# Kernel optimization log

Measured on AMD Instinct MI355X. Metric: run time of the kernel, lower is better.

## Reference

```python
import jax, jax.numpy as jnp
import numpy as np
import math

D_MODEL = 1024
NUM_HEADS = 16
HEAD_DIM = D_MODEL // NUM_HEADS
B, T = 2, 2048


def _linear_params(key, d_in, d_out):
    kw, kb = jax.random.split(key)
    s = 1.0 / math.sqrt(d_in)
    W = jax.random.uniform(kw, (d_in, d_out), jnp.float32, -s, s)
    b = jax.random.uniform(kb, (d_out,), jnp.float32, -s, s)
    return W, b


def setup_inputs() -> dict:
    key = jax.random.key(0)
    ks = jax.random.split(key, 10)
    x_real = jax.random.normal(ks[0], (B, T, D_MODEL), jnp.float32)
    x_imag = jax.random.normal(ks[1], (B, T, D_MODEL), jnp.float32)
    Wqr, bqr = _linear_params(ks[2], D_MODEL, D_MODEL)
    Wqi, bqi = _linear_params(ks[3], D_MODEL, D_MODEL)
    Wkr, bkr = _linear_params(ks[4], D_MODEL, D_MODEL)
    Wki, bki = _linear_params(ks[5], D_MODEL, D_MODEL)
    Wvr, bvr = _linear_params(ks[6], D_MODEL, D_MODEL)
    Wvi, bvi = _linear_params(ks[7], D_MODEL, D_MODEL)
    Wor, bor = _linear_params(ks[8], D_MODEL, D_MODEL)
    Woi, boi = _linear_params(ks[9], D_MODEL, D_MODEL)
    return dict(x_real=x_real, x_imag=x_imag,
                Wqr=Wqr, bqr=bqr, Wqi=Wqi, bqi=bqi,
                Wkr=Wkr, bkr=bkr, Wki=Wki, bki=bki,
                Wvr=Wvr, bvr=bvr, Wvi=Wvi, bvi=bvi,
                Wor=Wor, bor=bor, Woi=Woi, boi=boi)


def _heads(x):
    # (B,T,C) -> (B,H,T,Dh)
    b, t, _ = x.shape
    return x.reshape(b, t, NUM_HEADS, HEAD_DIM).transpose(0, 2, 1, 3)


def reference(x_real, x_imag,
              Wqr, bqr, Wqi, bqi, Wkr, bkr, Wki, bki,
              Wvr, bvr, Wvi, bvi, Wor, bor, Woi, boi):
    b, t, c = x_real.shape
    # NOTE: first two qr/qi assignments in the torch forward are dead code;
    # effective math is below.
    qr = _heads(x_real @ Wqr + bqr)
    qi = _heads(x_imag @ Wqi + bqi)
    kr = _heads(x_real @ Wkr + bkr)
    ki = _heads(x_imag @ Wki + bki)
    vr = _heads(x_real @ Wvr + bvr)
    vi = _heads(x_imag @ Wvi + bvi)
    # Re(Q K^H) score: Qr*Kr + Qi*Ki, scaled
    score = (jnp.einsum('bhtd,bhsd->bhts', qr, kr)
             + jnp.einsum('bhtd,bhsd->bhts', qi, ki)) / math.sqrt(HEAD_DIM)
    causal = jnp.triu(jnp.ones((t, t), dtype=bool), k=1)  # True above diagonal
    score = jnp.where(causal[None, None], -jnp.inf, score)
    attn = jax.nn.softmax(score, axis=-1)
    out_r = jnp.einsum('bhts,bhsd->bhtd', attn, vr).transpose(0, 2, 1, 3).reshape(b, t, c)
    out_i = jnp.einsum('bhts,bhsd->bhtd', attn, vi).transpose(0, 2, 1, 3).reshape(b, t, c)
    final_r = out_r @ Wor + bor
    final_i = out_i @ Woi + boi
    return (final_r, final_i)
```

## Files before the change

kernel.cpp:

```cpp
#include <hip/hip_runtime.h>
#include <hip/hip_bf16.h>


typedef __attribute__((ext_vector_type(8))) __bf16 bf16x8;
typedef __attribute__((ext_vector_type(4))) float f32x4;
typedef unsigned short u16;

#define L2E 1.44269504088896340736f

__device__ __forceinline__ void gl2lds16(const void* g, void* l) {
  __builtin_amdgcn_global_load_lds(
      (const __attribute__((address_space(1))) unsigned int*)g,
      (__attribute__((address_space(3))) unsigned int*)l, 16, 0, 0);
}

__device__ __forceinline__ u16 f2bf(float f) {
  union { float f; unsigned u; } v;
  v.f = f;
  unsigned r = v.u + 0x7FFFu + ((v.u >> 16) & 1u);
  return (u16)(r >> 16);
}

__global__ void cvt_bf16(const float* __restrict__ in, u16* __restrict__ out, int n) {
  int stride = gridDim.x * blockDim.x * 4;
  for (int i = (blockIdx.x * blockDim.x + threadIdx.x) * 4; i < n; i += stride) {
    float4 v = *(const float4*)(in + i);
    ushort4 o;
    o.x = f2bf(v.x); o.y = f2bf(v.y); o.z = f2bf(v.z); o.w = f2bf(v.w);
    *(ushort4*)(out + i) = o;
  }
}

struct WPtrs { const float* w[8]; };

__global__ void cvt_w_t(WPtrs ptrs, u16* __restrict__ out) {
  __shared__ float tile[32][33];
  const float* W = ptrs.w[blockIdx.z];
  u16* o = out + ((size_t)blockIdx.z << 20);
  int tx = threadIdx.x & 31, ty = threadIdx.x >> 5;
  int bx = blockIdx.x * 32, by = blockIdx.y * 32;
#pragma unroll
  for (int k = 0; k < 4; k++) {
    int r = by + ty + k * 8;
    tile[ty + k * 8][tx] = W[(size_t)r * 1024 + bx + tx];
  }
  __syncthreads();
#pragma unroll
  for (int k = 0; k < 4; k++) {
    int n = bx + ty + k * 8;
    o[(size_t)n * 1024 + by + tx] = f2bf(tile[tx][ty + k * 8]);
  }
}

struct GemmArgs {
  const u16* A[6];
  const u16* Wt[6];
  const float* bias[6];
  void* dst[6];
  int off[6];
};

template <int MODE>
__global__ __launch_bounds__(256, 2) void gemm_bf16(GemmArgs args) {
  const int z = blockIdx.z;
  const u16* __restrict__ A = args.A[z];
  const u16* __restrict__ Bt = args.Wt[z];
  const float* __restrict__ bias = args.bias[z];
  const int brow = blockIdx.x * 128;
  const int bcol = blockIdx.y * 128;

  __shared__ u16 lA[2][128 * 32];
  __shared__ u16 lB[2][128 * 32];

  const int tid = threadIdx.x;
  const int w = tid >> 6, lane = tid & 63;
  const int wrow = (w >> 1) * 64, wcol = (w & 1) * 64;

  f32x4 acc[4][4] = {};

  auto stage = [&](int buf, int t) {
    int k0 = t * 32;
#pragma unroll
    for (int s = 0; s < 2; s++) {
      int q = w * 2 + s;
      int lr = q * 16 + (lane >> 2);
      int csrc = (lane & 3) ^ ((lr >> 1) & 3);
      gl2lds16(A + (size_t)(brow + lr) * 1024 + k0 + csrc * 8, &lA[buf][q * 512]);
    }
#pragma unroll
    for (int s = 0; s < 2; s++) {
      int q = w * 2 + s;
      int lr = q * 16 + (lane >> 2);
      int csrc = (lane & 3) ^ ((lr >> 1) & 3);
      gl2lds16(Bt + (size_t)(bcol + lr) * 1024 + k0 + csrc * 8, &lB[buf][q * 512]);
    }
  };

  stage(0, 0);
  __syncthreads();

  int buf = 0;
  for (int t = 0; t < 32; t++) {
    if (t + 1 < 32) stage(buf ^ 1, t + 1);
    bf16x8 a[4], b[4];
#pragma unroll
    for (int i = 0; i < 4; i++) {
      int row = wrow + i * 16 + (lane & 15);
      int cs = (lane >> 4) ^ ((row >> 1) & 3);
      a[i] = *(const bf16x8*)&lA[buf][row * 32 + cs * 8];
      int col = wcol + i * 16 + (lane & 15);
      int cs2 = (lane >> 4) ^ ((col >> 1) & 3);
      b[i] = *(const bf16x8*)&lB[buf][col * 32 + cs2 * 8];
    }
#pragma unroll
    for (int i = 0; i < 4; i++)
#pragma unroll
      for (int j = 0; j < 4; j++)
        acc[i][j] = __builtin_amdgcn_mfma_f32_16x16x32_bf16(a[i], b[j], acc[i][j], 0, 0, 0);
    __syncthreads();
    buf ^= 1;
  }

  const int off = args.off[z];
#pragma unroll
  for (int i = 0; i < 4; i++)
#pragma unroll
    for (int j = 0; j < 4; j++)
#pragma unroll
      for (int r = 0; r < 4; r++) {
        int grow = brow + wrow + i * 16 + (lane >> 4) * 4 + r;
        int gcol = bcol + wcol + j * 16 + (lane & 15);
        float v = acc[i][j][r] + bias[gcol];
        if (MODE == 0) {
          ((float*)args.dst[z])[(size_t)grow * 1024 + gcol] = v;
        } else {
          int bb = grow >> 11, tt = grow & 2047;
          int h = gcol >> 6, dh = gcol & 63;
          ((u16*)args.dst[z])[(((size_t)(bb * 16 + h) * 2048 + tt) << 7) + off + dh] = f2bf(v);
        }
      }
}

__global__ void transpose_v(const u16* __restrict__ Vc, u16* __restrict__ Vt) {
  __shared__ u16 tile[64 * 64];
  const int bh = blockIdx.z, t0 = blockIdx.x * 64, d0 = blockIdx.y * 64;
  const int tid = threadIdx.x;
  const int tl = tid >> 3, c = tid & 7;
#pragma unroll
  for (int hh = 0; hh < 2; hh++) {
    int t = tl + hh * 32;
    int sc = c ^ (t & 7) ^ ((t >> 3) & 7);
    *(bf16x8*)&tile[t * 64 + sc * 8] =
        *(const bf16x8*)&Vc[((size_t)bh * 2048 + t0 + t) * 128 + d0 + c * 8];
  }
  __syncthreads();
#pragma unroll
  for (int hh = 0; hh < 2; hh++) {
    int d = tl + hh * 32;
    bf16x8 v;
#pragma unroll
    for (int j = 0; j < 8; j++) {
      int t = c * 8 + j;
      int sc = (d >> 3) ^ (t & 7) ^ ((t >> 3) & 7);
      v[j] = ((const __bf16*)tile)[t * 64 + sc * 8 + (d & 7)];
    }
    *(bf16x8*)&Vt[((size_t)bh * 128 + d0 + d) * 2048 + t0 + c * 8] = v;
  }
}

__global__ __launch_bounds__(256, 2) void attn_kernel(
    const u16* __restrict__ Q, const u16* __restrict__ K, const u16* __restrict__ Vt,
    u16* __restrict__ Or, u16* __restrict__ Oi) {
  const int bh = blockIdx.x;
  const int ii = (int)gridDim.y - 1 - (int)blockIdx.y;
  const int tid = threadIdx.x, w = tid >> 6, lane = tid & 63;
  const int ql = lane & 15, hi = lane >> 4;
  const int b = bh >> 4, h = bh & 15;

  __shared__ u16 lK[2][64 * 128];
  __shared__ u16 lV[2][128 * 64];
  __shared__ u16 lP[4][16 * 64];

  const int qrow0 = ii * 64 + w * 16;
  const int q = qrow0 + ql;

  bf16x8 qf[4];
#pragma unroll
  for (int kk = 0; kk < 4; kk++)
    qf[kk] = *(const bf16x8*)(Q + ((size_t)bh * 2048 + q) * 128 + kk * 32 + hi * 8);

  f32x4 o[8] = {};
  float m = -__builtin_inff(), l = 0.f;

  const int ntiles = ii + 1;

  auto stageKV = [&](int buf, int jt) {
#pragma unroll
    for (int s = 0; s < 4; s++) {
      int seg = w * 4 + s;
      int srow = seg * 4 + (lane >> 4);
      int csrc = (lane & 15) ^ (srow & 15);
      gl2lds16(K + ((size_t)bh * 2048 + jt * 64 + srow) * 128 + csrc * 8, &lK[buf][seg * 512]);
    }
#pragma unroll
    for (int s = 0; s < 4; s++) {
      int seg = w * 4 + s;
      int dv = seg * 8 + (lane >> 3);
      int csrc = (lane & 7) ^ (dv & 7);
      gl2lds16(Vt + ((size_t)bh * 128 + dv) * 2048 + jt * 64 + csrc * 8, &lV[buf][seg * 512]);
    }
  };

  stageKV(0, 0);
  __syncthreads();

  int buf = 0;
  for (int jt = 0; jt < ntiles; jt++) {
    if (jt + 1 < ntiles) stageKV(buf ^ 1, jt + 1);

    f32x4 s[4] = {};
#pragma unroll
    for (int kk = 0; kk < 4; kk++) {
#pragma unroll
      for (int j = 0; j < 4; j++) {
        int sl = j * 16 + ql;
        int cs = (kk * 4 + hi) ^ (sl & 15);
        bf16x8 kf = *(const bf16x8*)&lK[buf][sl * 128 + cs * 8];
        s[j] = __builtin_amdgcn_mfma_f32_16x16x32_bf16(kf, qf[kk], s[j], 0, 0, 0);
      }
    }

    const bool diag = (jt == ii);
    float mx = -__builtin_inff();
#pragma unroll
    for (int j = 0; j < 4; j++)
#pragma unroll
      for (int r = 0; r < 4; r++) {
        float v = s[j][r] * 0.125f;
        if (diag) {
          int kg = jt * 64 + j * 16 + hi * 4 + r;
          if (kg > q) v = -__builtin_inff();
        }
        s[j][r] = v;
        mx = fmaxf(mx, v);
      }
    mx = fmaxf(mx, __shfl_xor(mx, 16));
    mx = fmaxf(mx, __shfl_xor(mx, 32));

    if (__any(mx > m + 8.f)) {
      float mn = fmaxf(m, mx);
      float alpha = exp2f((m - mn) * L2E);
      l *= alpha;
#pragma unroll
      for (int jv = 0; jv < 8; jv++) o[jv] *= alpha;
      m = mn;
    }

    float rs = 0.f;
    unsigned pk[4][2];
#pragma unroll
    for (int j = 0; j < 4; j++) {
      float p0 = exp2f((s[j][0] - m) * L2E);
      float p1 = exp2f((s[j][1] - m) * L2E);
      float p2 = exp2f((s[j][2] - m) * L2E);
      float p3 = exp2f((s[j][3] - m) * L2E);
      rs += (p0 + p1) + (p2 + p3);
      pk[j][0] = (unsigned)f2bf(p0) | ((unsigned)f2bf(p1) << 16);
      pk[j][1] = (unsigned)f2bf(p2) | ((unsigned)f2bf(p3) << 16);
    }
    rs += __shfl_xor(rs, 16);
    rs += __shfl_xor(rs, 32);
    l += rs;

#pragma unroll
    for (int j = 0; j < 4; j++) {
      int byte_off = ql * 128 + ((j * 32 + hi * 8) ^ ((ql & 7) << 4));
      *(uint2*)((char*)&lP[w][0] + byte_off) = make_uint2(pk[j][0], pk[j][1]);
    }
    asm volatile("s_waitcnt lgkmcnt(0)" ::: "memory");
    __builtin_amdgcn_sched_barrier(0);

#pragma unroll
    for (int kks = 0; kks < 2; kks++) {
      int pb = ql * 128 + ((kks * 64 + hi * 16) ^ ((ql & 7) << 4));
      bf16x8 pf = *(const bf16x8*)((char*)&lP[w][0] + pb);
#pragma unroll
      for (int jv = 0; jv < 8; jv++) {
        int dv = jv * 16 + ql;
        int cs = (kks * 4 + hi) ^ (dv & 7);
        bf16x8 vf = *(const bf16x8*)&lV[buf][dv * 64 + cs * 8];
        o[jv] = __builtin_amdgcn_mfma_f32_16x16x32_bf16(vf, pf, o[jv], 0, 0, 0);
      }
    }

    __syncthreads();
    buf ^= 1;
  }

  float linv = 1.f / l;
  const size_t obase = ((size_t)b * 2048 + q) * 1024 + h * 64;
#pragma unroll
  for (int jv = 0; jv < 8; jv++) {
    ushort4 st;
    st.x = f2bf(o[jv][0] * linv);
    st.y = f2bf(o[jv][1] * linv);
    st.z = f2bf(o[jv][2] * linv);
    st.w = f2bf(o[jv][3] * linv);
    u16* dst = (jv < 4) ? Or : Oi;
    *(ushort4*)(dst + obase + (jv & 3) * 16 + hi * 4) = st;
  }
}

extern "C" void kernel_launch(void* const* d_in, const int* in_sizes, int n_in,
                              void* d_out, int out_size, void* d_ws, size_t ws_size,
                              hipStream_t stream) {
  (void)in_sizes; (void)n_in; (void)out_size; (void)ws_size;

  const float* x_real = (const float*)d_in[0];
  const float* x_imag = (const float*)d_in[1];

  char* ws = (char*)d_ws;
  size_t off = 0;
  auto alloc = [&](size_t bytes) {
    void* p = ws + off;
    off += (bytes + 255) & ~(size_t)255;
    return p;
  };
  const size_t MK = 4096ull * 1024;
  u16* xr16 = (u16*)alloc(MK * 2);
  u16* xi16 = (u16*)alloc(MK * 2);
  u16* Wt   = (u16*)alloc(8ull * 1024 * 1024 * 2);
  u16* Qc   = (u16*)alloc(32ull * 2048 * 128 * 2);
  u16* Kc   = (u16*)alloc(32ull * 2048 * 128 * 2);
  u16* Vc   = (u16*)alloc(32ull * 2048 * 128 * 2);
  u16* Vt   = (u16*)alloc(32ull * 2048 * 128 * 2);
  u16* Or   = Vc;
  u16* Oi   = Vc + MK;

  cvt_bf16<<<2048, 256, 0, stream>>>(x_real, xr16, (int)MK);
  cvt_bf16<<<2048, 256, 0, stream>>>(x_imag, xi16, (int)MK);

  WPtrs wp;
  wp.w[0] = (const float*)d_in[2];
  wp.w[1] = (const float*)d_in[4];
  wp.w[2] = (const float*)d_in[6];
  wp.w[3] = (const float*)d_in[8];
  wp.w[4] = (const float*)d_in[10];
  wp.w[5] = (const float*)d_in[12];
  wp.w[6] = (const float*)d_in[14];
  wp.w[7] = (const float*)d_in[16];
  cvt_w_t<<<dim3(32, 32, 8), 256, 0, stream>>>(wp, Wt);

  GemmArgs pa{};
  const u16* xs[2] = {xr16, xi16};
  for (int z = 0; z < 6; z++) {
    pa.A[z] = xs[z & 1];
    pa.Wt[z] = Wt + (size_t)z * 1048576;
    pa.off[z] = (z & 1) * 64;
  }
  pa.bias[0] = (const float*)d_in[3];
  pa.bias[1] = (const float*)d_in[5];
  pa.bias[2] = (const float*)d_in[7];
  pa.bias[3] = (const float*)d_in[9];
  pa.bias[4] = (const float*)d_in[11];
  pa.bias[5] = (const float*)d_in[13];
  pa.dst[0] = Qc; pa.dst[1] = Qc;
  pa.dst[2] = Kc; pa.dst[3] = Kc;
  pa.dst[4] = Vc; pa.dst[5] = Vc;
  gemm_bf16<1><<<dim3(32, 8, 6), 256, 0, stream>>>(pa);

  transpose_v<<<dim3(32, 2, 32), 256, 0, stream>>>(Vc, Vt);

  attn_kernel<<<dim3(32, 32), 256, 0, stream>>>(Qc, Kc, Vt, Or, Oi);

  GemmArgs fa{};
  fa.A[0] = Or; fa.A[1] = Oi;
  fa.Wt[0] = Wt + 6ull * 1048576;
  fa.Wt[1] = Wt + 7ull * 1048576;
  fa.bias[0] = (const float*)d_in[15];
  fa.bias[1] = (const float*)d_in[17];
  fa.dst[0] = (float*)d_out;
  fa.dst[1] = (float*)d_out + MK;
  fa.off[0] = 0; fa.off[1] = 0;
  gemm_bf16<0><<<dim3(32, 8, 2), 256, 0, stream>>>(fa);
}
```

Measured before the change: 195.7 us.

## Read V directly from global memory in attention and raise occupancy

Drops the LDS staging of V tiles in the attention kernel. Each lane now loads its V fragments straight from global (L2-cached) memory, which cuts LDS use from about 66KB to about 40KB per block, and launch bounds are raised to 4 blocks per CU. The 1/sqrt(d) score scale is folded into the Q projection GEMM epilogue, MFMA sections are wrapped in s_setprio, and bf16 packing uses native casts. The risk is that uncoalesced, unprefetched global V loads add latency on the PV matmul, and register pressure at 4 waves per SIMD may cause spills.

```diff
diff --git a/kernel.cpp b/kernel.cpp
--- a/kernel.cpp
+++ b/kernel.cpp
@@ -58,6 +58,7 @@
   const float* bias[6];
   void* dst[6];
   int off[6];
+  float scale[6];
 };
 
 template <int MODE>
@@ -122,6 +123,7 @@
   }
 
   const int off = args.off[z];
+  const float scl = args.scale[z];
 #pragma unroll
   for (int i = 0; i < 4; i++)
 #pragma unroll
@@ -130,7 +132,7 @@
       for (int r = 0; r < 4; r++) {
         int grow = brow + wrow + i * 16 + (lane >> 4) * 4 + r;
         int gcol = bcol + wcol + j * 16 + (lane & 15);
-        float v = acc[i][j][r] + bias[gcol];
+        float v = (acc[i][j][r] + bias[gcol]) * scl;
         if (MODE == 0) {
           ((float*)args.dst[z])[(size_t)grow * 1024 + gcol] = v;
         } else {
@@ -168,7 +170,7 @@
   }
 }
 
-__global__ __launch_bounds__(256, 2) void attn_kernel(
+__global__ __launch_bounds__(256, 4) void attn_kernel(
     const u16* __restrict__ Q, const u16* __restrict__ K, const u16* __restrict__ Vt,
     u16* __restrict__ Or, u16* __restrict__ Oi) {
   const int bh = blockIdx.x;
@@ -178,7 +180,6 @@
   const int b = bh >> 4, h = bh & 15;
 
   __shared__ u16 lK[2][64 * 128];
-  __shared__ u16 lV[2][128 * 64];
   __shared__ u16 lP[4][16 * 64];
 
   const int qrow0 = ii * 64 + w * 16;
@@ -189,12 +190,14 @@
   for (int kk = 0; kk < 4; kk++)
     qf[kk] = *(const bf16x8*)(Q + ((size_t)bh * 2048 + q) * 128 + kk * 32 + hi * 8);
 
+  const u16* Vrow = Vt + ((size_t)bh * 128 + ql) * 2048 + hi * 8;
+
   f32x4 o[8] = {};
   float m = -__builtin_inff(), l = 0.f;
 
   const int ntiles = ii + 1;
 
-  auto stageKV = [&](int buf, int jt) {
+  auto stageK = [&](int buf, int jt) {
 #pragma unroll
     for (int s = 0; s < 4; s++) {
       int seg = w * 4 + s;
@@ -202,23 +205,17 @@
       int csrc = (lane & 15) ^ (srow & 15);
       gl2lds16(K + ((size_t)bh * 2048 + jt * 64 + srow) * 128 + csrc * 8, &lK[buf][seg * 512]);
     }
-#pragma unroll
-    for (int s = 0; s < 4; s++) {
-      int seg = w * 4 + s;
-      int dv = seg * 8 + (lane >> 3);
-      int csrc = (lane & 7) ^ (dv & 7);
-      gl2lds16(Vt + ((size_t)bh * 128 + dv) * 2048 + jt * 64 + csrc * 8, &lV[buf][seg * 512]);
-    }
   };
 
-  stageKV(0, 0);
+  stageK(0, 0);
   __syncthreads();
 
   int buf = 0;
   for (int jt = 0; jt < ntiles; jt++) {
-    if (jt + 1 < ntiles) stageKV(buf ^ 1, jt + 1);
+    if (jt + 1 < ntiles) stageK(buf ^ 1, jt + 1);
 
     f32x4 s[4] = {};
+    __builtin_amdgcn_s_setprio(1);
 #pragma unroll
     for (int kk = 0; kk < 4; kk++) {
 #pragma unroll
@@ -229,6 +226,7 @@
         s[j] = __builtin_amdgcn_mfma_f32_16x16x32_bf16(kf, qf[kk], s[j], 0, 0, 0);
       }
     }
+    __builtin_amdgcn_s_setprio(0);
 
     const bool diag = (jt == ii);
     float mx = -__builtin_inff();
@@ -236,7 +234,7 @@
     for (int j = 0; j < 4; j++)
 #pragma unroll
       for (int r = 0; r < 4; r++) {
-        float v = s[j][r] * 0.125f;
+        float v = s[j][r];
         if (diag) {
           int kg = jt * 64 + j * 16 + hi * 4 + r;
           if (kg > q) v = -__builtin_inff();
@@ -257,7 +255,7 @@
     }
 
     float rs = 0.f;
-    unsigned pk[4][2];
+    uint2 pk[4];
 #pragma unroll
     for (int j = 0; j < 4; j++) {
       float p0 = exp2f((s[j][0] - m) * L2E);
@@ -265,8 +263,10 @@
       float p2 = exp2f((s[j][2] - m) * L2E);
       float p3 = exp2f((s[j][3] - m) * L2E);
       rs += (p0 + p1) + (p2 + p3);
-      pk[j][0] = (unsigned)f2bf(p0) | ((unsigned)f2bf(p1) << 16);
-      pk[j][1] = (unsigned)f2bf(p2) | ((unsigned)f2bf(p3) << 16);
+      union { __bf16 hh[4]; uint2 u; } cv;
+      cv.hh[0] = (__bf16)p0; cv.hh[1] = (__bf16)p1;
+      cv.hh[2] = (__bf16)p2; cv.hh[3] = (__bf16)p3;
+      pk[j] = cv.u;
     }
     rs += __shfl_xor(rs, 16);
     rs += __shfl_xor(rs, 32);
@@ -275,23 +275,23 @@
 #pragma unroll
     for (int j = 0; j < 4; j++) {
       int byte_off = ql * 128 + ((j * 32 + hi * 8) ^ ((ql & 7) << 4));
-      *(uint2*)((char*)&lP[w][0] + byte_off) = make_uint2(pk[j][0], pk[j][1]);
+      *(uint2*)((char*)&lP[w][0] + byte_off) = pk[j];
     }
     asm volatile("s_waitcnt lgkmcnt(0)" ::: "memory");
     __builtin_amdgcn_sched_barrier(0);
 
+    __builtin_amdgcn_s_setprio(1);
 #pragma unroll
     for (int kks = 0; kks < 2; kks++) {
       int pb = ql * 128 + ((kks * 64 + hi * 16) ^ ((ql & 7) << 4));
       bf16x8 pf = *(const bf16x8*)((char*)&lP[w][0] + pb);
 #pragma unroll
       for (int jv = 0; jv < 8; jv++) {
-        int dv = jv * 16 + ql;
-        int cs = (kks * 4 + hi) ^ (dv & 7);
-        bf16x8 vf = *(const bf16x8*)&lV[buf][dv * 64 + cs * 8];
+        bf16x8 vf = *(const bf16x8*)(Vrow + (size_t)jv * 32768 + jt * 64 + kks * 32);
         o[jv] = __builtin_amdgcn_mfma_f32_16x16x32_bf16(vf, pf, o[jv], 0, 0, 0);
       }
     }
+    __builtin_amdgcn_s_setprio(0);
 
     __syncthreads();
     buf ^= 1;
@@ -357,6 +357,7 @@
     pa.A[z] = xs[z & 1];
     pa.Wt[z] = Wt + (size_t)z * 1048576;
     pa.off[z] = (z & 1) * 64;
+    pa.scale[z] = (z < 2) ? 0.125f : 1.0f;
   }
   pa.bias[0] = (const float*)d_in[3];
   pa.bias[1] = (const float*)d_in[5];
@@ -382,5 +383,6 @@
   fa.dst[0] = (float*)d_out;
   fa.dst[1] = (float*)d_out + MK;
   fa.off[0] = 0; fa.off[1] = 0;
+  fa.scale[0] = 1.0f; fa.scale[1] = 1.0f;
   gemm_bf16<0><<<dim3(32, 8, 2), 256, 0, stream>>>(fa);
 }
```

New measurement: 292.9 us. 1.5x slower.

## Fold softmax scale into Q projection and trim attention inner-loop softmax work

Applied to the files above, without the earlier changes.

Moves the 1/sqrt(d) scaling of scores into the Q projection GEMM epilogue, so the attention loop no longer multiplies each score. The causal mask is applied only on the diagonal tile, and the cross-lane row max reduction now runs only when a rescale is triggered. The row-sum shuffles are deferred to the end of the loop, manual bf16 rounding is replaced with native bf16 conversion, and the MFMA sections are wrapped in s_setprio. Scaling Q before the bf16 cast is exact because 0.125 is a power of two. Deciding the rescale from a per-lane max before reduction still keeps the shared max consistent, since __any is wave-wide.

```diff
diff --git a/kernel.cpp b/kernel.cpp
--- a/kernel.cpp
+++ b/kernel.cpp
@@ -58,6 +58,7 @@
   const float* bias[6];
   void* dst[6];
   int off[6];
+  float scale[6];
 };
 
 template <int MODE>
@@ -122,6 +123,7 @@
   }
 
   const int off = args.off[z];
+  const float scl = args.scale[z];
 #pragma unroll
   for (int i = 0; i < 4; i++)
 #pragma unroll
@@ -130,7 +132,7 @@
       for (int r = 0; r < 4; r++) {
         int grow = brow + wrow + i * 16 + (lane >> 4) * 4 + r;
         int gcol = bcol + wcol + j * 16 + (lane & 15);
-        float v = acc[i][j][r] + bias[gcol];
+        float v = (acc[i][j][r] + bias[gcol]) * scl;
         if (MODE == 0) {
           ((float*)args.dst[z])[(size_t)grow * 1024 + gcol] = v;
         } else {
@@ -219,6 +221,7 @@
     if (jt + 1 < ntiles) stageKV(buf ^ 1, jt + 1);
 
     f32x4 s[4] = {};
+    __builtin_amdgcn_s_setprio(1);
 #pragma unroll
     for (int kk = 0; kk < 4; kk++) {
 #pragma unroll
@@ -229,25 +232,30 @@
         s[j] = __builtin_amdgcn_mfma_f32_16x16x32_bf16(kf, qf[kk], s[j], 0, 0, 0);
       }
     }
-
-    const bool diag = (jt == ii);
-    float mx = -__builtin_inff();
-#pragma unroll
-    for (int j = 0; j < 4; j++)
-#pragma unroll
-      for (int r = 0; r < 4; r++) {
-        float v = s[j][r] * 0.125f;
-        if (diag) {
+    __builtin_amdgcn_s_setprio(0);
+
+    if (jt == ii) {
+#pragma unroll
+      for (int j = 0; j < 4; j++)
+#pragma unroll
+        for (int r = 0; r < 4; r++) {
           int kg = jt * 64 + j * 16 + hi * 4 + r;
-          if (kg > q) v = -__builtin_inff();
+          if (kg > q) s[j][r] = -__builtin_inff();
         }
-        s[j][r] = v;
-        mx = fmaxf(mx, v);
-      }
-    mx = fmaxf(mx, __shfl_xor(mx, 16));
-    mx = fmaxf(mx, __shfl_xor(mx, 32));
+    }
+
+    float mx;
+    {
+      float a0 = fmaxf(fmaxf(s[0][0], s[0][1]), fmaxf(s[0][2], s[0][3]));
+      float a1 = fmaxf(fmaxf(s[1][0], s[1][1]), fmaxf(s[1][2], s[1][3]));
+      float a2 = fmaxf(fmaxf(s[2][0], s[2][1]), fmaxf(s[2][2], s[2][3]));
+      float a3 = fmaxf(fmaxf(s[3][0], s[3][1]), fmaxf(s[3][2], s[3][3]));
+      mx = fmaxf(fmaxf(a0, a1), fmaxf(a2, a3));
+    }
 
     if (__any(mx > m + 8.f)) {
+      mx = fmaxf(mx, __shfl_xor(mx, 16));
+      mx = fmaxf(mx, __shfl_xor(mx, 32));
       float mn = fmaxf(m, mx);
       float alpha = exp2f((m - mn) * L2E);
       l *= alpha;
@@ -256,30 +264,29 @@
       m = mn;
     }
 
-    float rs = 0.f;
-    unsigned pk[4][2];
+    uint2 pk[4];
 #pragma unroll
     for (int j = 0; j < 4; j++) {
       float p0 = exp2f((s[j][0] - m) * L2E);
       float p1 = exp2f((s[j][1] - m) * L2E);
       float p2 = exp2f((s[j][2] - m) * L2E);
       float p3 = exp2f((s[j][3] - m) * L2E);
-      rs += (p0 + p1) + (p2 + p3);
-      pk[j][0] = (unsigned)f2bf(p0) | ((unsigned)f2bf(p1) << 16);
-      pk[j][1] = (unsigned)f2bf(p2) | ((unsigned)f2bf(p3) << 16);
-    }
-    rs += __shfl_xor(rs, 16);
-    rs += __shfl_xor(rs, 32);
-    l += rs;
+      l += (p0 + p1) + (p2 + p3);
+      union { __bf16 hh[4]; uint2 u; } cv;
+      cv.hh[0] = (__bf16)p0; cv.hh[1] = (__bf16)p1;
+      cv.hh[2] = (__bf16)p2; cv.hh[3] = (__bf16)p3;
+      pk[j] = cv.u;
+    }
 
 #pragma unroll
     for (int j = 0; j < 4; j++) {
       int byte_off = ql * 128 + ((j * 32 + hi * 8) ^ ((ql & 7) << 4));
-      *(uint2*)((char*)&lP[w][0] + byte_off) = make_uint2(pk[j][0], pk[j][1]);
+      *(uint2*)((char*)&lP[w][0] + byte_off) = pk[j];
     }
     asm volatile("s_waitcnt lgkmcnt(0)" ::: "memory");
     __builtin_amdgcn_sched_barrier(0);
 
+    __builtin_amdgcn_s_setprio(1);
 #pragma unroll
     for (int kks = 0; kks < 2; kks++) {
       int pb = ql * 128 + ((kks * 64 + hi * 16) ^ ((ql & 7) << 4));
@@ -292,20 +299,25 @@
         o[jv] = __builtin_amdgcn_mfma_f32_16x16x32_bf16(vf, pf, o[jv], 0, 0, 0);
       }
     }
+    __builtin_amdgcn_s_setprio(0);
 
     __syncthreads();
     buf ^= 1;
   }
 
+  l += __shfl_xor(l, 16);
+  l += __shfl_xor(l, 32);
   float linv = 1.f / l;
   const size_t obase = ((size_t)b * 2048 + q) * 1024 + h * 64;
 #pragma unroll
   for (int jv = 0; jv < 8; jv++) {
     ushort4 st;
-    st.x = f2bf(o[jv][0] * linv);
-    st.y = f2bf(o[jv][1] * linv);
-    st.z = f2bf(o[jv][2] * linv);
-    st.w = f2bf(o[jv][3] * linv);
+    union { __bf16 hh[4]; ushort4 u; } cv;
+    cv.hh[0] = (__bf16)(o[jv][0] * linv);
+    cv.hh[1] = (__bf16)(o[jv][1] * linv);
+    cv.hh[2] = (__bf16)(o[jv][2] * linv);
+    cv.hh[3] = (__bf16)(o[jv][3] * linv);
+    st = cv.u;
     u16* dst = (jv < 4) ? Or : Oi;
     *(ushort4*)(dst + obase + (jv & 3) * 16 + hi * 4) = st;
   }
@@ -357,6 +369,7 @@
     pa.A[z] = xs[z & 1];
     pa.Wt[z] = Wt + (size_t)z * 1048576;
     pa.off[z] = (z & 1) * 64;
+    pa.scale[z] = (z < 2) ? 0.125f : 1.0f;
   }
   pa.bias[0] = (const float*)d_in[3];
   pa.bias[1] = (const float*)d_in[5];
@@ -382,5 +395,6 @@
   fa.dst[0] = (float*)d_out;
   fa.dst[1] = (float*)d_out + MK;
   fa.off[0] = 0; fa.off[1] = 0;
+  fa.scale[0] = 1.0f; fa.scale[1] = 1.0f;
   gemm_bf16<0><<<dim3(32, 8, 2), 256, 0, stream>>>(fa);
 }
```

Result: faster. 188.6 us (-3.6%).
